# Optimization experiments

Hardware: AMD Instinct MI355X
Metric: run time of the kernel (lower is better)

## Reference

```python
import jax, jax.numpy as jnp
import numpy as np

D_MODEL = 1024
NUM_HEADS = 16
HEAD_DIM = D_MODEL // NUM_HEADS


def setup_inputs() -> dict:
    key = jax.random.key(0)
    k_x, k_wqkv, k_bqkv, k_wo, k_bo = jax.random.split(key, 5)
    x = jax.random.normal(k_x, (2, 2048, D_MODEL), dtype=jnp.float32)
    s = 1.0 / np.sqrt(D_MODEL)
    W_qkv = jax.random.uniform(k_wqkv, (D_MODEL, 3 * D_MODEL), jnp.float32, -s, s)
    b_qkv = jax.random.uniform(k_bqkv, (3 * D_MODEL,), jnp.float32, -s, s)
    W_o = jax.random.uniform(k_wo, (D_MODEL, D_MODEL), jnp.float32, -s, s)
    b_o = jax.random.uniform(k_bo, (D_MODEL,), jnp.float32, -s, s)
    return {"x": x, "W_qkv": W_qkv, "b_qkv": b_qkv, "W_o": W_o, "b_o": b_o}


def reference(x, W_qkv, b_qkv, W_o, b_o):
    B, S, D = x.shape
    # fused QKV projection: [B,S,3D]
    qkv = jnp.einsum('bsd,de->bse', x, W_qkv) + b_qkv
    # [B,S,H,3*hd] -> [B,H,S,3*hd]
    qkv = qkv.reshape(B, S, NUM_HEADS, 3 * HEAD_DIM).transpose(0, 2, 1, 3)
    q, k, v = jnp.split(qkv, 3, axis=-1)  # each [B,H,S,hd]
    scale = 1.0 / jnp.sqrt(jnp.asarray(HEAD_DIM, dtype=x.dtype))
    scores = jnp.einsum('bhqd,bhkd->bhqk', q, k) * scale  # [B,H,S,S]
    attn = jax.nn.softmax(scores, axis=-1)
    values = jnp.einsum('bhqk,bhkd->bhqd', attn, v)  # [B,H,S,hd]
    values = values.transpose(0, 2, 1, 3).reshape(B, S, D)
    out = jnp.einsum('bsd,de->bse', values, W_o) + b_o
    return out
```

## Files before the change

kernel.cpp:

```cpp
#include <hip/hip_runtime.h>
#include <stdint.h>
#include <stddef.h>

typedef _Float16 f16;
typedef _Float16 f16x8 __attribute__((ext_vector_type(8)));
typedef _Float16 f16x4 __attribute__((ext_vector_type(4)));
typedef float    f32x2 __attribute__((ext_vector_type(2)));
typedef float    f32x4 __attribute__((ext_vector_type(4)));
typedef float    f32x16 __attribute__((ext_vector_type(16)));
typedef int      i32x4 __attribute__((ext_vector_type(4)));
typedef int      i32x2 __attribute__((ext_vector_type(2)));

#define S_LEN 2048
#define DM    1024
#define NH    16
#define HD    64
#define NTOK  4096
#define NQKV  3072
#define QSCALE 0.18033688011112042f

#if __has_builtin(__builtin_amdgcn_exp2f)
#define EXP2(x) __builtin_amdgcn_exp2f(x)
#else
#define EXP2(x) __expf((x) * 0.69314718055994531f)
#endif

__device__ __forceinline__ void gl_lds16(const void* g, void* l) {
  __builtin_amdgcn_global_load_lds(
      (const __attribute__((address_space(1))) void*)g,
      (__attribute__((address_space(3))) void*)l, 16, 0, 0);
}

__device__ __forceinline__ void pl32_swap(int& a, int& b) {
#if __has_builtin(__builtin_amdgcn_permlane32_swap)
  i32x2 r = __builtin_amdgcn_permlane32_swap(a, b, false, false);
  a = r.x; b = r.y;
#else
  asm volatile("v_permlane32_swap_b32 %0, %1" : "+v"(a), "+v"(b));
#endif
}

__device__ __forceinline__ float swap_half(float x, int hi) {
  int a = __builtin_bit_cast(int, x);
  int b = a;
  pl32_swap(a, b);
  return __builtin_bit_cast(float, hi ? a : b);
}

__device__ __forceinline__ int pkrtz(float a, float b) {
  auto h = __builtin_amdgcn_cvt_pkrtz(a, b);
  return __builtin_bit_cast(int, h);
}

__device__ __forceinline__ f16x8 mk_frag(int a, int b, int c, int d) {
  i32x4 v = {a, b, c, d};
  return __builtin_bit_cast(f16x8, v);
}

__device__ __forceinline__ f32x2 pk2(const f32x16& v, int i) {
  f32x2 r = {v[2*i], v[2*i+1]};
  return r;
}

__global__ __launch_bounds__(256) void cvt_all_kernel(
    const float* __restrict__ x,    f16* __restrict__ x_h,
    const float* __restrict__ Wqkv, f16* __restrict__ Wqkv_t,
    const float* __restrict__ Wo,   f16* __restrict__ Wo_t)
{
  __shared__ float t[32][33];
  const int b = blockIdx.x, tid = threadIdx.x;
  if (b < 2048) {
    int i = (b * 256 + tid) * 8;
    float4 a0 = *(const float4*)(x + i);
    float4 a1 = *(const float4*)(x + i + 4);
    f16x8 v = {(f16)a0.x,(f16)a0.y,(f16)a0.z,(f16)a0.w,(f16)a1.x,(f16)a1.y,(f16)a1.z,(f16)a1.w};
    *(f16x8*)(x_h + i) = v;
    return;
  }
  const float* in; f16* out; int R, C, c0, r0;
  if (b < 5120) {
    int tt = b - 2048; in = Wqkv; out = Wqkv_t; R = DM; C = NQKV;
    c0 = (tt % 96) * 32; r0 = (tt / 96) * 32;
  } else {
    int tt = b - 5120; in = Wo; out = Wo_t; R = DM; C = DM;
    c0 = (tt & 31) * 32; r0 = (tt >> 5) * 32;
  }
  int tx = tid & 31, ty = tid >> 5;
  #pragma unroll
  for (int i = 0; i < 4; ++i)
    t[ty + i*8][tx] = in[(size_t)(r0 + ty + i*8) * C + c0 + tx];
  __syncthreads();
  #pragma unroll
  for (int i = 0; i < 4; ++i)
    out[(size_t)(c0 + ty + i*8) * R + r0 + tx] = (f16)t[tx][ty + i*8];
}

template<int EPI>
__global__ __launch_bounds__(256) void gemm128_kernel(
    const f16* __restrict__ A, const f16* __restrict__ Bt,
    const float* __restrict__ bias,
    f16* __restrict__ qb, f16* __restrict__ kb, f16* __restrict__ vtb,
    float* __restrict__ out)
{
  __shared__ f16 As[128*32];
  __shared__ f16 Bs[128*32];
  const int tid = threadIdx.x;
  const int wid = tid >> 6, lane = tid & 63;
  const int g = lane >> 4, r = lane & 15;
  const int flat = blockIdx.x;
  const int xcd = flat & 7, idx = flat >> 3;
  const int m0 = (xcd * 4 + (idx & 3)) * 128;
  const int n0 = (idx >> 2) * 128;
  const int wm = (wid >> 1) * 64, wn = (wid & 1) * 64;

  f32x4 acc[4][4] = {};
  const int srow = tid >> 2;
  const int sch  = tid & 3;

  for (int kt = 0; kt < DM/32; ++kt) {
    const int k0 = kt * 32;
    __syncthreads();
    #pragma unroll
    for (int c = 0; c < 2; ++c) {
      int row = c*64 + srow;
      int sw = (sch ^ ((row >> 1) & 3)) * 8;
      gl_lds16(A  + (size_t)(m0 + row) * DM + k0 + sw, (char*)As + c*4096 + tid*16);
      gl_lds16(Bt + (size_t)(n0 + row) * DM + k0 + sw, (char*)Bs + c*4096 + tid*16);
    }
    __syncthreads();
    f16x8 a[4], b[4];
    #pragma unroll
    for (int mt = 0; mt < 4; ++mt) {
      int rl = wm + mt*16 + r;
      a[mt] = *(const f16x8*)(As + rl*32 + ((g ^ ((rl >> 1) & 3)) * 8));
    }
    #pragma unroll
    for (int nt = 0; nt < 4; ++nt) {
      int cl = wn + nt*16 + r;
      b[nt] = *(const f16x8*)(Bs + cl*32 + ((g ^ ((cl >> 1) & 3)) * 8));
    }
    #pragma unroll
    for (int mt = 0; mt < 4; ++mt)
      #pragma unroll
      for (int nt = 0; nt < 4; ++nt)
        acc[mt][nt] = __builtin_amdgcn_mfma_f32_16x16x32_f16(a[mt], b[nt], acc[mt][nt], 0, 0, 0);
  }

  if (EPI == 0) {
    #pragma unroll
    for (int mt = 0; mt < 4; ++mt) {
      int row0 = m0 + wm + mt*16 + g*4;
      int b_ = row0 >> 11, s0 = row0 & 2047;
      #pragma unroll
      for (int nt = 0; nt < 4; ++nt) {
        int col = n0 + wn + nt*16 + r;
        float bv = bias[col];
        int h = col / 192;
        int cc = col - h*192;
        int which = cc >> 6, d = cc & 63;
        size_t bh = (size_t)(b_*NH + h);
        if (which == 2) {
          f16x4 v;
          #pragma unroll
          for (int i = 0; i < 4; ++i) v[i] = (f16)(acc[mt][nt][i] + bv);
          *(f16x4*)(vtb + (bh*HD + d)*S_LEN + s0) = v;
        } else if (which == 0) {
          #pragma unroll
          for (int i = 0; i < 4; ++i)
            qb[(bh*S_LEN + s0 + i)*HD + d] = (f16)((acc[mt][nt][i] + bv) * QSCALE);
        } else {
          #pragma unroll
          for (int i = 0; i < 4; ++i)
            kb[(bh*S_LEN + s0 + i)*HD + d] = (f16)(acc[mt][nt][i] + bv);
        }
      }
    }
  } else {
    #pragma unroll
    for (int mt = 0; mt < 4; ++mt) {
      int row0 = m0 + wm + mt*16 + g*4;
      #pragma unroll
      for (int nt = 0; nt < 4; ++nt) {
        int col = n0 + wn + nt*16 + r;
        float bv = bias[col];
        #pragma unroll
        for (int i = 0; i < 4; ++i)
          out[(size_t)(row0 + i)*DM + col] = acc[mt][nt][i] + bv;
      }
    }
  }
}

__global__ __launch_bounds__(512) void attn_kernel(
    const f16* __restrict__ qb, const f16* __restrict__ kb,
    const f16* __restrict__ vtb, f16* __restrict__ values)
{
  __shared__ __align__(16) char smem[67584];

  const int tid = threadIdx.x;
  const int wid = tid >> 6, lane = tid & 63;
  const int wq = wid & 3, wk = wid >> 2;
  const int ql = lane & 31, hi = lane >> 5;
  const int flat = blockIdx.x;
  const int xcd = flat & 7, idx = flat >> 3;
  const int bh = xcd * 4 + (idx & 3);
  const int q0 = (idx >> 2) * 256 + wq * 64;
  const f16* qh = qb  + (size_t)bh * S_LEN * HD;
  const f16* kh = kb  + (size_t)bh * S_LEN * HD;
  const f16* vh = vtb + (size_t)bh * HD * S_LEN;
  const int kbase0 = wk * 1024;
  const int htid = tid & 255;

  int koff[2], voff[2];
  #pragma unroll
  for (int c = 0; c < 2; ++c) {
    int ca = htid + c*256, pr = ca >> 4, pc = ca & 15, lc = pc ^ (pr & 15);
    int row2 = pr*2 + (lc >> 3), e8 = (lc & 7) * 8;
    koff[c] = row2 * HD + e8;
    voff[c] = row2 * S_LEN + e8;
  }

  f16x8 qfA[4], qfB[4];
  #pragma unroll
  for (int dk = 0; dk < 4; ++dk) {
    qfA[dk] = *(const f16x8*)(qh + (size_t)(q0 + ql)*HD + dk*16 + hi*8);
    qfB[dk] = *(const f16x8*)(qh + (size_t)(q0 + 32 + ql)*HD + dk*16 + hi*8);
  }

  const int r0b = (ql >> 1) << 8;
  const int xv  = (ql >> 1) & 15;
  const int hb  = ((ql & 1) << 3) | hi;

  f32x2 laccA = {0.f, 0.f}, laccB = {0.f, 0.f};
  f32x16 oA0 = {}, oA1 = {}, oB0 = {}, oB1 = {};
  f32x16 sA0, sA1, sB0, sB1;
  const f32x16 ZERO = {};

  #define STAGE(kt_, buf_) do {                                            \
    const f16* ks_ = kh + (size_t)(kbase0 + (kt_)*64) * HD;                \
    const f16* vs_ = vh + (kbase0 + (kt_)*64);                             \
    char* kd_ = smem + (wk*2 + (buf_))*8192;                               \
    char* vd_ = smem + 32768 + (wk*2 + (buf_))*8192;                       \
    gl_lds16(ks_ + koff[0], kd_ + htid*16);                                \
    gl_lds16(ks_ + koff[1], kd_ + 4096 + htid*16);                         \
    gl_lds16(vs_ + voff[0], vd_ + htid*16);                                \
    gl_lds16(vs_ + voff[1], vd_ + 4096 + htid*16);                         \
  } while (0)

  #define QK_STEP(buf_) do {                                               \
    const char* KsC = smem + (wk*2 + (buf_))*8192;                         \
    {                                                                      \
      int off0 = r0b + ((hb ^ xv) << 4);                                   \
      f16x8 kf0 = *(const f16x8*)(KsC + off0);                             \
      f16x8 kf1 = *(const f16x8*)(KsC + 4096 + off0);                      \
      sA0 = __builtin_amdgcn_mfma_f32_32x32x16_f16(kf0, qfA[0], ZERO, 0, 0, 0); \
      sB0 = __builtin_amdgcn_mfma_f32_32x32x16_f16(kf0, qfB[0], ZERO, 0, 0, 0); \
      sA1 = __builtin_amdgcn_mfma_f32_32x32x16_f16(kf1, qfA[0], ZERO, 0, 0, 0); \
      sB1 = __builtin_amdgcn_mfma_f32_32x32x16_f16(kf1, qfB[0], ZERO, 0, 0, 0); \
    }                                                                      \
    _Pragma("unroll")                                                      \
    for (int dk = 1; dk < 4; ++dk) {                                       \
      int off = r0b + (((hb | (dk << 1)) ^ xv) << 4);                      \
      f16x8 kf0 = *(const f16x8*)(KsC + off);                              \
      f16x8 kf1 = *(const f16x8*)(KsC + 4096 + off);                       \
      sA0 = __builtin_amdgcn_mfma_f32_32x32x16_f16(kf0, qfA[dk], sA0, 0, 0, 0); \
      sB0 = __builtin_amdgcn_mfma_f32_32x32x16_f16(kf0, qfB[dk], sB0, 0, 0, 0); \
      sA1 = __builtin_amdgcn_mfma_f32_32x32x16_f16(kf1, qfA[dk], sA1, 0, 0, 0); \
      sB1 = __builtin_amdgcn_mfma_f32_32x32x16_f16(kf1, qfB[dk], sB1, 0, 0, 0); \
    }                                                                      \
  } while (0)

  #define EXP_H(S_, LACC_, PFA_, PFB_) do {                                \
    _Pragma("unroll")                                                      \
    for (int i = 0; i < 16; ++i) S_[i] = EXP2(S_[i]);                      \
    f32x2 sm[4];                                                           \
    _Pragma("unroll")                                                      \
    for (int i = 0; i < 4; ++i) sm[i] = pk2(S_, i) + pk2(S_, i + 4);       \
    sm[0] += sm[1]; sm[2] += sm[3]; LACC_ += sm[0] + sm[2];                \
    int a = pkrtz(S_[0], S_[1]), b = pkrtz(S_[2], S_[3]);                  \
    int c = pkrtz(S_[4], S_[5]), d = pkrtz(S_[6], S_[7]);                  \
    pl32_swap(a, c); pl32_swap(b, d);                                      \
    PFA_ = mk_frag(a, b, c, d);                                            \
    a = pkrtz(S_[8],  S_[9]);  b = pkrtz(S_[10], S_[11]);                  \
    c = pkrtz(S_[12], S_[13]); d = pkrtz(S_[14], S_[15]);                  \
    pl32_swap(a, c); pl32_swap(b, d);                                      \
    PFB_ = mk_frag(a, b, c, d);                                            \
  } while (0)

  #define PV_STEP(buf_) do {                                               \
    const char* VsC = smem + 32768 + (wk*2 + (buf_))*8192;                 \
    _Pragma("unroll")                                                      \
    for (int w = 0; w < 4; ++w) {                                          \
      int off = r0b + (((hb | (w << 1)) ^ xv) << 4);                       \
      f16x8 vf0 = *(const f16x8*)(VsC + off);                              \
      f16x8 vf1 = *(const f16x8*)(VsC + 4096 + off);                       \
      oA0 = __builtin_amdgcn_mfma_f32_32x32x16_f16(pfA[w], vf0, oA0, 0, 0, 0); \
      oA1 = __builtin_amdgcn_mfma_f32_32x32x16_f16(pfA[w], vf1, oA1, 0, 0, 0); \
      oB0 = __builtin_amdgcn_mfma_f32_32x32x16_f16(pfB[w], vf0, oB0, 0, 0, 0); \
      oB1 = __builtin_amdgcn_mfma_f32_32x32x16_f16(pfB[w], vf1, oB1, 0, 0, 0); \
    }                                                                      \
  } while (0)

  f16x8 pfA[4], pfB[4];
  STAGE(0, 0);
  __syncthreads();

  for (int kt = 0; kt < 16; ++kt) {
    const int cur = kt & 1;
    if (kt + 1 < 16) STAGE(kt + 1, cur ^ 1);
    QK_STEP(cur);
    EXP_H(sA0, laccA, pfA[0], pfA[1]);
    EXP_H(sA1, laccA, pfA[2], pfA[3]);
    EXP_H(sB0, laccB, pfB[0], pfB[1]);
    EXP_H(sB1, laccB, pfB[2], pfB[3]);
    PV_STEP(cur);
    __syncthreads();
  }
  #undef STAGE
  #undef QK_STEP
  #undef EXP_H
  #undef PV_STEP

  float lA = laccA.x + laccA.y;  lA += swap_half(lA, hi);
  float lB = laccB.x + laccB.y;  lB += swap_half(lB, hi);

  const int slot = wq*64 + lane;
  float* lpl = (float*)(smem + 65536);
  float* ipl = (float*)(smem + 66560);
  if (wk == 1) {
    #pragma unroll
    for (int t = 0; t < 4; ++t) {
      *(f32x4*)(smem + (0*8 + 0*4 + t)*4096 + slot*16) = (f32x4){oA0[4*t], oA0[4*t+1], oA0[4*t+2], oA0[4*t+3]};
      *(f32x4*)(smem + (0*8 + 1*4 + t)*4096 + slot*16) = (f32x4){oA1[4*t], oA1[4*t+1], oA1[4*t+2], oA1[4*t+3]};
      *(f32x4*)(smem + (1*8 + 0*4 + t)*4096 + slot*16) = (f32x4){oB0[4*t], oB0[4*t+1], oB0[4*t+2], oB0[4*t+3]};
      *(f32x4*)(smem + (1*8 + 1*4 + t)*4096 + slot*16) = (f32x4){oB1[4*t], oB1[4*t+1], oB1[4*t+2], oB1[4*t+3]};
    }
    lpl[wq*64 + 0*32 + ql] = lA;
    lpl[wq*64 + 1*32 + ql] = lB;
  }
  __syncthreads();
  if (wk == 0) {
    float invA = 1.0f / (lA + lpl[wq*64 + ql]);
    float invB = 1.0f / (lB + lpl[wq*64 + 32 + ql]);
    ipl[wq*64 + ql]      = invA;
    ipl[wq*64 + 32 + ql] = invB;
  }
  __syncthreads();
  if (wk == 0) {
    const int b_ = bh >> 4, h = bh & 15;
    #pragma unroll
    for (int g2 = 0; g2 < 2; ++g2) {
      const f32x16& s0 = g2 ? oB0 : oA0;
      const f32x16& s1 = g2 ? oB1 : oA1;
      #pragma unroll
      for (int t = 0; t < 4; ++t) {
        f32x4 p0 = *(const f32x4*)(smem + (g2*8 + 0*4 + t)*4096 + slot*16);
        f32x4 p1 = *(const f32x4*)(smem + (g2*8 + 1*4 + t)*4096 + slot*16);
        f32x4 iv = *(const f32x4*)(ipl + wq*64 + g2*32 + 4*hi + 8*t);
        #pragma unroll
        for (int i = 0; i < 4; ++i) {
          int qrow = q0 + g2*32 + 4*hi + 8*t + i;
          size_t base = (size_t)(b_*S_LEN + qrow) * DM + h*HD + ql;
          values[base]      = (f16)((s0[4*t+i] + p0[i]) * iv[i]);
          values[base + 32] = (f16)((s1[4*t+i] + p1[i]) * iv[i]);
        }
      }
    }
  }
}

extern "C" void kernel_launch(void* const* d_in, const int* in_sizes, int n_in,
                              void* d_out, int out_size, void* d_ws, size_t ws_size,
                              hipStream_t stream) {
  (void)in_sizes; (void)n_in; (void)out_size; (void)ws_size;
  const float* x    = (const float*)d_in[0];
  const float* Wqkv = (const float*)d_in[1];
  const float* bqkv = (const float*)d_in[2];
  const float* Wo   = (const float*)d_in[3];
  const float* bo   = (const float*)d_in[4];
  float* out = (float*)d_out;

  char* ws = (char*)d_ws;
  f16* x_h    = (f16*)(ws);
  f16* Wqkv_t = (f16*)(ws + ( 8ull<<20));
  f16* Wo_t   = (f16*)(ws + (14ull<<20));
  f16* qbuf   = (f16*)(ws + (16ull<<20));
  f16* kbuf   = (f16*)(ws + (24ull<<20));
  f16* vtbuf  = (f16*)(ws + (32ull<<20));
  f16* vals   = (f16*)(ws + (40ull<<20));

  cvt_all_kernel<<<dim3(6144), dim3(256), 0, stream>>>(
      x, x_h, Wqkv, Wqkv_t, Wo, Wo_t);

  gemm128_kernel<0><<<dim3(768), dim3(256), 0, stream>>>(
      x_h, Wqkv_t, bqkv, qbuf, kbuf, vtbuf, nullptr);

  attn_kernel<<<dim3(256), dim3(512), 0, stream>>>(qbuf, kbuf, vtbuf, vals);

  gemm128_kernel<1><<<dim3(256), dim3(256), 0, stream>>>(
      vals, Wo_t, bo, nullptr, nullptr, nullptr, out);
}
```

Baseline: 108.0 us.

## Load K and V fragments directly from global memory instead of LDS staging

Removes the double-buffered global-to-LDS staging of K and V tiles, and the per-iteration __syncthreads, from the attention loop. Each wave now reads its K and V MFMA fragments straight from global memory, relying on L1/L2 caching for reuse across the four q-waves that share a tile. This drops the barrier and LDS traffic but adds redundant global loads and exposes their latency, since there is no longer any prefetch of the next tile.

```diff
diff --git a/kernel.cpp b/kernel.cpp
--- a/kernel.cpp
+++ b/kernel.cpp
@@ -209,16 +209,6 @@
   const f16* kh = kb  + (size_t)bh * S_LEN * HD;
   const f16* vh = vtb + (size_t)bh * HD * S_LEN;
   const int kbase0 = wk * 1024;
-  const int htid = tid & 255;
-
-  int koff[2], voff[2];
-  #pragma unroll
-  for (int c = 0; c < 2; ++c) {
-    int ca = htid + c*256, pr = ca >> 4, pc = ca & 15, lc = pc ^ (pr & 15);
-    int row2 = pr*2 + (lc >> 3), e8 = (lc & 7) * 8;
-    koff[c] = row2 * HD + e8;
-    voff[c] = row2 * S_LEN + e8;
-  }
 
   f16x8 qfA[4], qfB[4];
   #pragma unroll
@@ -227,48 +217,10 @@
     qfB[dk] = *(const f16x8*)(qh + (size_t)(q0 + 32 + ql)*HD + dk*16 + hi*8);
   }
 
-  const int r0b = (ql >> 1) << 8;
-  const int xv  = (ql >> 1) & 15;
-  const int hb  = ((ql & 1) << 3) | hi;
-
   f32x2 laccA = {0.f, 0.f}, laccB = {0.f, 0.f};
   f32x16 oA0 = {}, oA1 = {}, oB0 = {}, oB1 = {};
   f32x16 sA0, sA1, sB0, sB1;
   const f32x16 ZERO = {};
-
-  #define STAGE(kt_, buf_) do {                                            \
-    const f16* ks_ = kh + (size_t)(kbase0 + (kt_)*64) * HD;                \
-    const f16* vs_ = vh + (kbase0 + (kt_)*64);                             \
-    char* kd_ = smem + (wk*2 + (buf_))*8192;                               \
-    char* vd_ = smem + 32768 + (wk*2 + (buf_))*8192;                       \
-    gl_lds16(ks_ + koff[0], kd_ + htid*16);                                \
-    gl_lds16(ks_ + koff[1], kd_ + 4096 + htid*16);                         \
-    gl_lds16(vs_ + voff[0], vd_ + htid*16);                                \
-    gl_lds16(vs_ + voff[1], vd_ + 4096 + htid*16);                         \
-  } while (0)
-
-  #define QK_STEP(buf_) do {                                               \
-    const char* KsC = smem + (wk*2 + (buf_))*8192;                         \
-    {                                                                      \
-      int off0 = r0b + ((hb ^ xv) << 4);                                   \
-      f16x8 kf0 = *(const f16x8*)(KsC + off0);                             \
-      f16x8 kf1 = *(const f16x8*)(KsC + 4096 + off0);                      \
-      sA0 = __builtin_amdgcn_mfma_f32_32x32x16_f16(kf0, qfA[0], ZERO, 0, 0, 0); \
-      sB0 = __builtin_amdgcn_mfma_f32_32x32x16_f16(kf0, qfB[0], ZERO, 0, 0, 0); \
-      sA1 = __builtin_amdgcn_mfma_f32_32x32x16_f16(kf1, qfA[0], ZERO, 0, 0, 0); \
-      sB1 = __builtin_amdgcn_mfma_f32_32x32x16_f16(kf1, qfB[0], ZERO, 0, 0, 0); \
-    }                                                                      \
-    _Pragma("unroll")                                                      \
-    for (int dk = 1; dk < 4; ++dk) {                                       \
-      int off = r0b + (((hb | (dk << 1)) ^ xv) << 4);                      \
-      f16x8 kf0 = *(const f16x8*)(KsC + off);                              \
-      f16x8 kf1 = *(const f16x8*)(KsC + 4096 + off);                       \
-      sA0 = __builtin_amdgcn_mfma_f32_32x32x16_f16(kf0, qfA[dk], sA0, 0, 0, 0); \
-      sB0 = __builtin_amdgcn_mfma_f32_32x32x16_f16(kf0, qfB[dk], sB0, 0, 0, 0); \
-      sA1 = __builtin_amdgcn_mfma_f32_32x32x16_f16(kf1, qfA[dk], sA1, 0, 0, 0); \
-      sB1 = __builtin_amdgcn_mfma_f32_32x32x16_f16(kf1, qfB[dk], sB1, 0, 0, 0); \
-    }                                                                      \
-  } while (0)
 
   #define EXP_H(S_, LACC_, PFA_, PFB_) do {                                \
     _Pragma("unroll")                                                      \
@@ -287,39 +239,46 @@
     PFB_ = mk_frag(a, b, c, d);                                            \
   } while (0)
 
-  #define PV_STEP(buf_) do {                                               \
-    const char* VsC = smem + 32768 + (wk*2 + (buf_))*8192;                 \
-    _Pragma("unroll")                                                      \
-    for (int w = 0; w < 4; ++w) {                                          \
-      int off = r0b + (((hb | (w << 1)) ^ xv) << 4);                       \
-      f16x8 vf0 = *(const f16x8*)(VsC + off);                              \
-      f16x8 vf1 = *(const f16x8*)(VsC + 4096 + off);                       \
-      oA0 = __builtin_amdgcn_mfma_f32_32x32x16_f16(pfA[w], vf0, oA0, 0, 0, 0); \
-      oA1 = __builtin_amdgcn_mfma_f32_32x32x16_f16(pfA[w], vf1, oA1, 0, 0, 0); \
-      oB0 = __builtin_amdgcn_mfma_f32_32x32x16_f16(pfB[w], vf0, oB0, 0, 0, 0); \
-      oB1 = __builtin_amdgcn_mfma_f32_32x32x16_f16(pfB[w], vf1, oB1, 0, 0, 0); \
-    }                                                                      \
-  } while (0)
-
   f16x8 pfA[4], pfB[4];
-  STAGE(0, 0);
-  __syncthreads();
 
   for (int kt = 0; kt < 16; ++kt) {
-    const int cur = kt & 1;
-    if (kt + 1 < 16) STAGE(kt + 1, cur ^ 1);
-    QK_STEP(cur);
+    const f16* kbase = kh + (size_t)(kbase0 + kt*64) * HD;
+    const f16* vbase = vh + kbase0 + kt*64;
+
+    {
+      f16x8 kf0 = *(const f16x8*)(kbase + (size_t)ql*HD + hi*8);
+      f16x8 kf1 = *(const f16x8*)(kbase + (size_t)(32 + ql)*HD + hi*8);
+      sA0 = __builtin_amdgcn_mfma_f32_32x32x16_f16(kf0, qfA[0], ZERO, 0, 0, 0);
+      sB0 = __builtin_amdgcn_mfma_f32_32x32x16_f16(kf0, qfB[0], ZERO, 0, 0, 0);
+      sA1 = __builtin_amdgcn_mfma_f32_32x32x16_f16(kf1, qfA[0], ZERO, 0, 0, 0);
+      sB1 = __builtin_amdgcn_mfma_f32_32x32x16_f16(kf1, qfB[0], ZERO, 0, 0, 0);
+    }
+    #pragma unroll
+    for (int dk = 1; dk < 4; ++dk) {
+      f16x8 kf0 = *(const f16x8*)(kbase + (size_t)ql*HD + dk*16 + hi*8);
+      f16x8 kf1 = *(const f16x8*)(kbase + (size_t)(32 + ql)*HD + dk*16 + hi*8);
+      sA0 = __builtin_amdgcn_mfma_f32_32x32x16_f16(kf0, qfA[dk], sA0, 0, 0, 0);
+      sB0 = __builtin_amdgcn_mfma_f32_32x32x16_f16(kf0, qfB[dk], sB0, 0, 0, 0);
+      sA1 = __builtin_amdgcn_mfma_f32_32x32x16_f16(kf1, qfA[dk], sA1, 0, 0, 0);
+      sB1 = __builtin_amdgcn_mfma_f32_32x32x16_f16(kf1, qfB[dk], sB1, 0, 0, 0);
+    }
+
     EXP_H(sA0, laccA, pfA[0], pfA[1]);
     EXP_H(sA1, laccA, pfA[2], pfA[3]);
     EXP_H(sB0, laccB, pfB[0], pfB[1]);
     EXP_H(sB1, laccB, pfB[2], pfB[3]);
-    PV_STEP(cur);
-    __syncthreads();
-  }
-  #undef STAGE
-  #undef QK_STEP
+
+    #pragma unroll
+    for (int w = 0; w < 4; ++w) {
+      f16x8 vf0 = *(const f16x8*)(vbase + (size_t)ql*S_LEN + w*16 + hi*8);
+      f16x8 vf1 = *(const f16x8*)(vbase + (size_t)(32 + ql)*S_LEN + w*16 + hi*8);
+      oA0 = __builtin_amdgcn_mfma_f32_32x32x16_f16(pfA[w], vf0, oA0, 0, 0, 0);
+      oA1 = __builtin_amdgcn_mfma_f32_32x32x16_f16(pfA[w], vf1, oA1, 0, 0, 0);
+      oB0 = __builtin_amdgcn_mfma_f32_32x32x16_f16(pfB[w], vf0, oB0, 0, 0, 0);
+      oB1 = __builtin_amdgcn_mfma_f32_32x32x16_f16(pfB[w], vf1, oB1, 0, 0, 0);
+    }
+  }
   #undef EXP_H
-  #undef PV_STEP
 
   float lA = laccA.x + laccA.y;  lA += swap_half(lA, hi);
   float lB = laccB.x + laccB.y;  lB += swap_half(lB, hi);
```

Measured after the change: 131.2 us. 21.5% more time.
